# Kernel optimization log

Measured on AMD Instinct MI355X. Metric: run time of the kernel, lower is better.

## Reference

```python
import jax, jax.numpy as jnp
import numpy as np

N_STATE = 4      # d_state from CrossMambaFusionBlock(d_state=4)
DT_RANK = 48     # ceil(768/16), standard Mamba dt_rank='auto'
D_CONV = 4       # depthwise causal conv kernel size


def _ln(x, g, b):
    m = jnp.mean(x, axis=-1, keepdims=True)
    v = jnp.mean((x - m) ** 2, axis=-1, keepdims=True)
    return (x - m) * jax.lax.rsqrt(v + 1e-5) * g + b


def _dwconv1d(u, w, b):
    # u: (B,L,D); w: (D,1,K) depthwise causal conv along token dim L
    K = w.shape[-1]
    up = jnp.pad(jnp.transpose(u, (0, 2, 1)), ((0, 0), (0, 0), (K - 1, 0)))
    out = jax.lax.conv_general_dilated(up, w, (1,), 'VALID',
                                       feature_group_count=w.shape[0],
                                       dimension_numbers=('NCH', 'OIH', 'NCH'))
    return jnp.transpose(out, (0, 2, 1)) + b


def _pre(x, g, b, Win, Wconv, bconv, Wxp, Wdt, bdt):
    # LayerNorm -> in_proj -> depthwise conv + SiLU -> dt/B/C projections
    B_, H, W, C = x.shape
    xn = _ln(x, g, b).reshape(B_, H * W, C)
    u, z = jnp.split(xn @ Win, 2, axis=-1)              # (B,L,D) each
    u = jax.nn.silu(_dwconv1d(u, Wconv, bconv))
    dbl = u @ Wxp                                        # (B,L,R+2N)
    dtr, Bm, Cm = jnp.split(dbl, [DT_RANK, DT_RANK + N_STATE], axis=-1)
    dt = jax.nn.softplus(dtr @ Wdt + bdt)                # (B,L,D)
    return u, z, dt, Bm, Cm


def _selective_scan(u, dt, Alog, Bm, Cm, Dskip):
    # u, dt: (B,L,D); Alog: (D,N); Bm, Cm: (B,L,N)
    A = -jnp.exp(Alog)
    dA = jnp.exp(dt[..., None] * A)                      # (B,L,D,N) decay
    dBu = (dt * u)[..., None] * Bm[:, :, None, :]        # (B,L,D,N) input

    def comb(c1, c2):
        a1, h1 = c1
        a2, h2 = c2
        return a1 * a2, a2 * h1 + h2

    _, h = jax.lax.associative_scan(comb, (dA, dBu), axis=1)
    return jnp.einsum('bldn,bln->bld', h, Cm) + u * Dskip


def _forward(x1, x2,
             ln_g1, ln_b1, Win1, Wconv1, bconv1, Wxp1, Wdt1, bdt1, Alog1, Dskip1, Wout1,
             ln_g2, ln_b2, Win2, Wconv2, bconv2, Wxp2, Wdt2, bdt2, Alog2, Dskip2, Wout2):
    x1 = jnp.transpose(x1, (0, 2, 3, 1))  # BCHW -> BHWC (as in forward_features)
    x2 = jnp.transpose(x2, (0, 2, 3, 1))
    B_, H, W, C = x1.shape
    u1, z1, dt1, B1, C1 = _pre(x1, ln_g1, ln_b1, Win1, Wconv1, bconv1, Wxp1, Wdt1, bdt1)
    u2, z2, dt2, B2, C2 = _pre(x2, ln_g2, ln_b2, Win2, Wconv2, bconv2, Wxp2, Wdt2, bdt2)
    # Cross-modal fusion: each stream's SSM state is read out with the OTHER
    # stream's C projection (cross selective scan).
    y1 = _selective_scan(u1, dt1, Alog1, B1, C2, Dskip1)
    y2 = _selective_scan(u2, dt2, Alog2, B2, C1, Dskip2)
    o1 = ((y1 * jax.nn.silu(z1)) @ Wout1).reshape(B_, H, W, C)
    o2 = ((y2 * jax.nn.silu(z2)) @ Wout2).reshape(B_, H, W, C)
    return x1 + o1, x2 + o2


def setup_inputs():
    key = jax.random.key(0)
    ks = jax.random.split(key, 16)
    B_, C, H, W = 2, 768, 64, 64
    D = C  # d_inner (ssm_ratio = 1)

    def nrm(k, shape, s=0.02):
        return jax.random.normal(k, shape, jnp.float32) * s

    inp = {
        'x1': jax.random.normal(ks[0], (B_, C, H, W), jnp.float32),
        'x2': jax.random.normal(ks[1], (B_, C, H, W), jnp.float32),
    }
    for i, o in ((1, 2), (2, 8)):
        inp[f'ln_g{i}'] = jnp.ones((C,), jnp.float32)
        inp[f'ln_b{i}'] = jnp.zeros((C,), jnp.float32)
        inp[f'Win{i}'] = nrm(ks[o], (C, 2 * D))
        inp[f'Wconv{i}'] = nrm(ks[o + 1], (D, 1, D_CONV), 0.1)
        inp[f'bconv{i}'] = jnp.zeros((D,), jnp.float32)
        inp[f'Wxp{i}'] = nrm(ks[o + 2], (D, DT_RANK + 2 * N_STATE))
        inp[f'Wdt{i}'] = nrm(ks[o + 3], (DT_RANK, D), 0.05)
        inp[f'bdt{i}'] = jnp.full((D,), -4.6, jnp.float32)  # softplus -> dt ~ 0.01
        inp[f'Alog{i}'] = jnp.log(jnp.broadcast_to(
            jnp.arange(1, N_STATE + 1, dtype=jnp.float32), (D, N_STATE)))
        inp[f'Dskip{i}'] = jnp.ones((D,), jnp.float32)
        inp[f'Wout{i}'] = nrm(ks[o + 4], (D, C))
    return inp


def reference(x1, x2,
              ln_g1, ln_b1, Win1, Wconv1, bconv1, Wxp1, Wdt1, bdt1, Alog1, Dskip1, Wout1,
              ln_g2, ln_b2, Win2, Wconv2, bconv2, Wxp2, Wdt2, bdt2, Alog2, Dskip2, Wout2):
    return _forward(x1, x2,
                    ln_g1, ln_b1, Win1, Wconv1, bconv1, Wxp1, Wdt1, bdt1, Alog1, Dskip1, Wout1,
                    ln_g2, ln_b2, Win2, Wconv2, bconv2, Wxp2, Wdt2, bdt2, Alog2, Dskip2, Wout2)
```

## Files before the change

kernel.cpp:

```cpp
#include <hip/hip_runtime.h>
#include <cmath>

#define LDIM 4096
#define CDIM 768
#define BDIM 2
#define NST 4
#define RNK 48
#define CH 64
#define LC 64
#define NDT 896

typedef short bf16x8 __attribute__((ext_vector_type(8)));
typedef float f32x4 __attribute__((ext_vector_type(4)));

__device__ __forceinline__ float sigmoidf_(float x) { return 1.f / (1.f + __expf(-x)); }

__device__ __forceinline__ unsigned short f2bf(float f) {
    unsigned int u = __float_as_uint(f);
    u += 0x7fffu + ((u >> 16) & 1u);
    return (unsigned short)(u >> 16);
}
__device__ __forceinline__ float bf2f(unsigned short us) {
    unsigned int u = ((unsigned int)us) << 16;
    return __uint_as_float(u);
}
__device__ __forceinline__ float bf2f_lo(unsigned int p) { return __uint_as_float(p << 16); }
__device__ __forceinline__ float bf2f_hi(unsigned int p) { return __uint_as_float(p & 0xffff0000u); }

__device__ __forceinline__ void llds16(const unsigned short* g, unsigned short* l) {
    __builtin_amdgcn_global_load_lds(
        (const __attribute__((address_space(1))) unsigned int*)g,
        (__attribute__((address_space(3))) unsigned int*)l, 16, 0, 0);
}

__global__ __launch_bounds__(256) void prep_kernel(
    const float* __restrict__ x0, const float* __restrict__ x1, float* __restrict__ stats,
    const float* __restrict__ Win0, const float* __restrict__ Win1,
    const float* __restrict__ Wout0, const float* __restrict__ Wout1,
    unsigned short* __restrict__ WinT0, unsigned short* __restrict__ WinT1,
    unsigned short* __restrict__ WoutT0, unsigned short* __restrict__ WoutT1,
    const float* __restrict__ Wxp0, const float* __restrict__ Wdt0,
    const float* __restrict__ Wxp1, const float* __restrict__ Wdt1,
    unsigned short* __restrict__ Wc0, unsigned short* __restrict__ Wc1)
{
    __shared__ float smem[64 * 65];
    int bid = blockIdx.x;
    int t = threadIdx.x;

    if (bid < 256) {
        int s = bid >> 7;
        int b = (bid >> 6) & 1;
        int l0 = (bid & 63) * 64;
        int wave = t >> 6, lane = t & 63;
        const float* x = s ? x1 : x0;
        const float* xp = x + ((size_t)b * CDIM) * LDIM + l0 + lane;
        float sm = 0.f, sq = 0.f;
        int cbeg = wave * 192;
#pragma unroll
        for (int i0 = 0; i0 < 192; i0 += 16) {
            float v[16];
#pragma unroll
            for (int j = 0; j < 16; j++) v[j] = xp[(size_t)(cbeg + i0 + j) * LDIM];
#pragma unroll
            for (int j = 0; j < 16; j++) { sm += v[j]; sq += v[j] * v[j]; }
        }
        float* red = smem;
        red[(0 * 4 + wave) * 64 + lane] = sm;
        red[(1 * 4 + wave) * 64 + lane] = sq;
        __syncthreads();
        if (wave == 0) {
            float s_ = red[lane] + red[64 + lane] + red[128 + lane] + red[192 + lane];
            float q_ = red[256 + lane] + red[320 + lane] + red[384 + lane] + red[448 + lane];
            float m = s_ * (1.f / CDIM);
            float var = q_ * (1.f / CDIM) - m * m;
            int idx = s * 8192 + b * LDIM + l0 + lane;
            stats[2 * idx] = m;
            stats[2 * idx + 1] = rsqrtf(var + 1e-5f);
        }
        return;
    }
    if (bid < 1408) {
        int b2 = bid - 256;
        int bx = b2 % 24, by = (b2 / 24) % 12, z = b2 / 288;
        const float* W = (z == 0) ? Win0 : (z == 1) ? Win1 : (z == 2) ? Wout0 : Wout1;
        unsigned short* Wt = (z == 0) ? WinT0 : (z == 1) ? WinT1 : (z == 2) ? WoutT0 : WoutT1;
        const int K = CDIM;
        const int N = (z < 2) ? 2 * CDIM : CDIM;
        if (bx * 64 >= N) return;
        float (*tile)[65] = (float(*)[65])smem;
        int n0 = bx * 64, k0 = by * 64;
        int tn = t & 63, tg = t >> 6;
#pragma unroll
        for (int i = 0; i < 16; i++) {
            int kl = tg * 16 + i;
            tile[kl][tn] = W[(size_t)(k0 + kl) * N + n0 + tn];
        }
        __syncthreads();
#pragma unroll
        for (int i = 0; i < 16; i++) {
            int nl = tg * 16 + i;
            int k = k0 + tn, n = n0 + nl;
            Wt[(size_t)n * K + k] = f2bf(tile[tn][nl]);
        }
        return;
    }
    {
        int b3 = bid - 1408;
        int bx = b3 % 12, by = (b3 / 12) % 14, s = b3 / 168;
        const float* Wxp = s ? Wxp1 : Wxp0;
        const float* Wdt = s ? Wdt1 : Wdt0;
        unsigned short* WcombT = s ? Wc1 : Wc0;
        int k = bx * 64 + (t & 63);
        int n0 = by * 64;
        float wx[RNK];
#pragma unroll
        for (int r = 0; r < RNK; r++) wx[r] = Wxp[k * 56 + r];
        for (int i = (t >> 6); i < 64; i += 4) {
            int n = n0 + i;
            float val;
            if (n < CDIM) {
                float acc = 0.f;
#pragma unroll
                for (int r = 0; r < RNK; r++) acc += wx[r] * Wdt[(size_t)r * CDIM + n];
                val = acc;
            } else if (n < CDIM + 8) {
                val = Wxp[k * 56 + RNK + (n - CDIM)];
            } else {
                val = 0.f;
            }
            WcombT[(size_t)n * CDIM + k] = f2bf(val);
        }
    }
}

__global__ __launch_bounds__(256) void transpose_ln_kernel(
    const float* __restrict__ x0, const float* __restrict__ x1,
    const float* __restrict__ g0, const float* __restrict__ bb0,
    const float* __restrict__ g1, const float* __restrict__ bb1,
    const float* __restrict__ stats,
    unsigned short* __restrict__ xnb0, unsigned short* __restrict__ xnb1,
    float* __restrict__ out)
{
    __shared__ float tile[64][65];
    int t = threadIdx.x;
    int c0 = blockIdx.x * 64, l0 = blockIdx.y * 64;
    int z = blockIdx.z;
    int s = z >> 1, b = z & 1;
    const float* x = s ? x1 : x0;
    const float* g = s ? g1 : g0;
    const float* bb = s ? bb1 : bb0;
    unsigned short* xnb = s ? xnb1 : xnb0;
    int lane16 = t & 15, cg = t >> 4;
#pragma unroll
    for (int i = 0; i < 4; i++) {
        int cl = cg + 16 * i;
        f32x4 v = *(const f32x4*)&x[((size_t)(b * CDIM + c0 + cl)) * LDIM + l0 + lane16 * 4];
#pragma unroll
        for (int j = 0; j < 4; j++) tile[cl][lane16 * 4 + j] = v[j];
    }
    __syncthreads();
    const size_t SZ = (size_t)BDIM * LDIM * CDIM;
    int tl = t & 63, tg = t >> 6;
#pragma unroll
    for (int i = 0; i < 16; i++) {
        int ll = tg * 16 + i;
        int l = l0 + ll, c = c0 + tl;
        float v = tile[tl][ll];
        int sidx = s * 8192 + b * LDIM + l;
        float m = stats[sidx * 2], rs = stats[sidx * 2 + 1];
        size_t o = ((size_t)(b * LDIM + l)) * CDIM + c;
        out[(size_t)s * SZ + o] = v;
        xnb[o] = f2bf((v - m) * rs * g[c] + bb[c]);
    }
}

__global__ __launch_bounds__(512, 4) void gemm_mfma(
    const unsigned short* __restrict__ A0, const unsigned short* __restrict__ A1,
    const unsigned short* __restrict__ Bt0, const unsigned short* __restrict__ Bt1,
    void* __restrict__ C0, void* __restrict__ C1, int ldc, int K, int epi,
    const float* __restrict__ bias0, const float* __restrict__ bias1,
    float* __restrict__ D0, float* __restrict__ D1)
{
    const unsigned short* A = blockIdx.z ? A1 : A0;
    const unsigned short* Bt = blockIdx.z ? Bt1 : Bt0;
    void* C = blockIdx.z ? C1 : C0;
    const float* bias = blockIdx.z ? bias1 : bias0;
    float* D = blockIdx.z ? D1 : D0;

    __shared__ unsigned short As[3][128 * 32];
    __shared__ unsigned short Bs[3][128 * 32];
    const int tid = threadIdx.x;
    const int wave = tid >> 6, lane = tid & 63;
    const int row0 = blockIdx.x * 128, col0 = blockIdx.y * 128;
    const int wm = (wave >> 2) * 64, wn = (wave & 3) * 32;
    f32x4 acc[4][2] = {};
    const int lr = lane >> 2;
    const int gi = ((lane & 3) ^ ((lane >> 3) & 3)) * 8;
    const int fr = lane & 15, fc = lane >> 4;

    const unsigned short* ga0 = A + (size_t)(row0 + wave * 16 + lr) * K + gi;
    const unsigned short* gb0 = Bt + (size_t)(col0 + wave * 16 + lr) * K + gi;
    const int rb = wave * 16;

#define ISSUE(st, kb)                         \
    do {                                      \
        llds16(ga0 + (kb), &As[st][rb * 32]); \
        llds16(gb0 + (kb), &Bs[st][rb * 32]); \
    } while (0)

    const int NIT = K / 32;
    ISSUE(0, 0);
    ISSUE(1, 32);
    for (int i = 0; i < NIT; i++) {
        if (i < NIT - 1) __builtin_amdgcn_s_waitcnt(0xF72);
        else __builtin_amdgcn_s_waitcnt(0xF70);
        __builtin_amdgcn_s_barrier();
        if (i + 2 < NIT) ISSUE((i + 2) % 3, (i + 2) * 32);
        const unsigned short* as = As[i % 3];
        const unsigned short* bs = Bs[i % 3];
        bf16x8 af[4], bfr[2];
#pragma unroll
        for (int ii = 0; ii < 4; ii++) {
            int r = wm + ii * 16 + fr;
            af[ii] = *(const bf16x8*)&as[r * 32 + (fc ^ ((r >> 1) & 3)) * 8];
        }
#pragma unroll
        for (int j = 0; j < 2; j++) {
            int r = wn + j * 16 + fr;
            bfr[j] = *(const bf16x8*)&bs[r * 32 + (fc ^ ((r >> 1) & 3)) * 8];
        }
#pragma unroll
        for (int ii = 0; ii < 4; ii++)
#pragma unroll
            for (int j = 0; j < 2; j++)
                acc[ii][j] = __builtin_amdgcn_mfma_f32_16x16x32_bf16(af[ii], bfr[j], acc[ii][j], 0, 0, 0);
    }
#undef ISSUE

    const int cr = (lane >> 4) * 4, cc = lane & 15;
#pragma unroll
    for (int ii = 0; ii < 4; ii++)
#pragma unroll
        for (int j = 0; j < 2; j++) {
            int col = col0 + wn + j * 16 + cc;
#pragma unroll
            for (int r = 0; r < 4; r++) {
                int row = row0 + wm + ii * 16 + cr + r;
                float v = acc[ii][j][r];
                if (epi == 1) {
                    float* Cf = (float*)C;
                    size_t o = (size_t)row * ldc + col;
                    Cf[o] = v + Cf[o];
                } else if (epi == 2) {
                    if (col < CDIM) {
                        v += bias[col];
                        v = (v > 20.f) ? v : __logf(1.f + __expf(v));
                        ((unsigned short*)C)[(size_t)row * ldc + col] = f2bf(v);
                    } else if (col < CDIM + 8) {
                        D[(size_t)row * 8 + (col - CDIM)] = v;
                    }
                } else {
                    ((unsigned short*)C)[(size_t)row * ldc + col] = f2bf(v);
                }
            }
        }
}

__global__ __launch_bounds__(256) void conv_silu_kernel(
    const unsigned short* __restrict__ uzb0, const unsigned short* __restrict__ uzb1,
    const float* __restrict__ w0, const float* __restrict__ bc0,
    const float* __restrict__ w1, const float* __restrict__ bc1,
    unsigned short* __restrict__ ub0, unsigned short* __restrict__ ub1)
{
    int s = blockIdx.y;
    const unsigned short* uzb = s ? uzb1 : uzb0;
    const float* w = s ? w1 : w0;
    const float* bc = s ? bc1 : bc0;
    unsigned short* ub = s ? ub1 : ub0;
    int idx = blockIdx.x * 256 + threadIdx.x;
    int d8 = (idx % 96) * 8;
    int bl = idx / 96;
    int l = bl & (LDIM - 1);

    float wr[8][4];
#pragma unroll
    for (int q = 0; q < 8; q++) {
        f32x4 wv = *(const f32x4*)&w[(d8 + q) * 4];
#pragma unroll
        for (int k = 0; k < 4; k++) wr[q][k] = wv[k];
    }
    float acc[8];
    f32x4 b0 = *(const f32x4*)&bc[d8];
    f32x4 b1 = *(const f32x4*)&bc[d8 + 4];
#pragma unroll
    for (int q = 0; q < 4; q++) { acc[q] = b0[q]; acc[4 + q] = b1[q]; }

#pragma unroll
    for (int k = 0; k < 4; k++) {
        int ls = l - 3 + k;
        if (ls >= 0) {
            bf16x8 uv = *(const bf16x8*)&uzb[(size_t)(bl - 3 + k) * (2 * CDIM) + d8];
#pragma unroll
            for (int q = 0; q < 8; q++)
                acc[q] += bf2f((unsigned short)uv[q]) * wr[q][k];
        }
    }
    bf16x8 ov;
#pragma unroll
    for (int q = 0; q < 8; q++) {
        float v = acc[q];
        ov[q] = (short)f2bf(v * sigmoidf_(v));
    }
    *(bf16x8*)&ub[(size_t)bl * CDIM + d8] = ov;
}

__global__ __launch_bounds__(256) void scan_phaseA(
    const unsigned short* __restrict__ u0, const unsigned short* __restrict__ dt0,
    const float* __restrict__ dbl0, const float* __restrict__ Alog0,
    const unsigned short* __restrict__ u1, const unsigned short* __restrict__ dt1,
    const float* __restrict__ dbl1, const float* __restrict__ Alog1,
    float* __restrict__ agg)
{
    int idx = blockIdx.x * 256 + threadIdx.x;
    int dp = idx % 384;
    int d0 = dp * 2;
    int t1 = idx / 384;
    int c = t1 % CH;
    int t2 = t1 / CH;
    int b = t2 & 1;
    int s = t2 >> 1;
    const unsigned short* u = s ? u1 : u0;
    const unsigned short* dt = s ? dt1 : dt0;
    const float* dbl = s ? dbl1 : dbl0;
    const float* Alog = s ? Alog1 : Alog0;
    float A[2][4];
#pragma unroll
    for (int j = 0; j < 2; j++)
#pragma unroll
        for (int n = 0; n < 4; n++) A[j][n] = -__expf(Alog[(d0 + j) * 4 + n]);
    float h[2][4] = {}, aa[2][4];
#pragma unroll
    for (int j = 0; j < 2; j++)
#pragma unroll
        for (int n = 0; n < 4; n++) aa[j][n] = 1.f;
    int rowb = b * LDIM + c * LC;
    for (int t = 0; t < LC; t++) {
        int row = rowb + t;
        unsigned int up = *(const unsigned int*)&u[(size_t)row * CDIM + d0];
        unsigned int dp2 = *(const unsigned int*)&dt[(size_t)row * CDIM + d0];
        float uv[2] = {bf2f_lo(up), bf2f_hi(up)};
        float dtv[2] = {bf2f_lo(dp2), bf2f_hi(dp2)};
        const float* bm = dbl + (size_t)row * 8;
#pragma unroll
        for (int j = 0; j < 2; j++) {
            float du = dtv[j] * uv[j];
#pragma unroll
            for (int n = 0; n < 4; n++) {
                float dA = __expf(dtv[j] * A[j][n]);
                h[j][n] = dA * h[j][n] + du * bm[n];
                aa[j][n] *= dA;
            }
        }
    }
    size_t base = ((size_t)(s * 2 + b) * CH + c) * CDIM + d0;
#pragma unroll
    for (int j = 0; j < 2; j++) {
        float* o = agg + (base + j) * 8;
#pragma unroll
        for (int n = 0; n < 4; n++) { o[n] = aa[j][n]; o[4 + n] = h[j][n]; }
    }
}

__global__ __launch_bounds__(256) void scan_phaseB(const float* __restrict__ agg,
                                                   float* __restrict__ hinit)
{
    int idx = blockIdx.x * 256 + threadIdx.x;
    int d = idx % CDIM;
    int sb = idx / CDIM;
    float st[4] = {0, 0, 0, 0};
    for (int c = 0; c < CH; c++) {
        size_t base = ((size_t)sb * CH + c) * CDIM + d;
        const float* a = agg + base * 8;
        float* hi = hinit + base * 4;
#pragma unroll
        for (int n = 0; n < 4; n++) hi[n] = st[n];
#pragma unroll
        for (int n = 0; n < 4; n++) st[n] = a[n] * st[n] + a[4 + n];
    }
}

__global__ __launch_bounds__(256) void scan_phaseC(
    const unsigned short* __restrict__ u0, const unsigned short* __restrict__ dt0,
    const unsigned short* __restrict__ uzb0, const float* __restrict__ dbl0,
    const float* __restrict__ Alog0, const float* __restrict__ Dsk0, unsigned short* __restrict__ g0,
    const unsigned short* __restrict__ u1, const unsigned short* __restrict__ dt1,
    const unsigned short* __restrict__ uzb1, const float* __restrict__ dbl1,
    const float* __restrict__ Alog1, const float* __restrict__ Dsk1, unsigned short* __restrict__ g1,
    const float* __restrict__ hinit)
{
    int idx = blockIdx.x * 256 + threadIdx.x;
    int dp = idx % 384;
    int d0 = dp * 2;
    int t1 = idx / 384;
    int c = t1 % CH;
    int t2 = t1 / CH;
    int b = t2 & 1;
    int s = t2 >> 1;
    const unsigned short* u = s ? u1 : u0;
    const unsigned short* dt = s ? dt1 : dt0;
    const unsigned short* uzb = s ? uzb1 : uzb0;
    const float* dbl = s ? dbl1 : dbl0;
    const float* dblO = s ? dbl0 : dbl1;
    const float* Alog = s ? Alog1 : Alog0;
    const float* Dsk = s ? Dsk1 : Dsk0;
    unsigned short* gated = s ? g1 : g0;
    float A[2][4];
#pragma unroll
    for (int j = 0; j < 2; j++)
#pragma unroll
        for (int n = 0; n < 4; n++) A[j][n] = -__expf(Alog[(d0 + j) * 4 + n]);
    float Dv[2] = {Dsk[d0], Dsk[d0 + 1]};
    float h[2][4];
    size_t base = ((size_t)(s * 2 + b) * CH + c) * CDIM + d0;
#pragma unroll
    for (int j = 0; j < 2; j++) {
        const float* hi = hinit + (base + j) * 4;
#pragma unroll
        for (int n = 0; n < 4; n++) h[j][n] = hi[n];
    }
    int rowb = b * LDIM + c * LC;
    for (int t = 0; t < LC; t++) {
        int row = rowb + t;
        unsigned int up = *(const unsigned int*)&u[(size_t)row * CDIM + d0];
        unsigned int dp2 = *(const unsigned int*)&dt[(size_t)row * CDIM + d0];
        unsigned int zp = *(const unsigned int*)&uzb[(size_t)row * (2 * CDIM) + CDIM + d0];
        float uv[2] = {bf2f_lo(up), bf2f_hi(up)};
        float dtv[2] = {bf2f_lo(dp2), bf2f_hi(dp2)};
        float zv[2] = {bf2f_lo(zp), bf2f_hi(zp)};
        const float* bm = dbl + (size_t)row * 8;
        const float* cm = dblO + (size_t)row * 8 + 4;
        unsigned int outp = 0;
#pragma unroll
        for (int j = 0; j < 2; j++) {
            float du = dtv[j] * uv[j];
            float y = 0.f;
#pragma unroll
            for (int n = 0; n < 4; n++) {
                float dA = __expf(dtv[j] * A[j][n]);
                h[j][n] = dA * h[j][n] + du * bm[n];
                y += h[j][n] * cm[n];
            }
            y += uv[j] * Dv[j];
            unsigned short gb = f2bf(y * (zv[j] * sigmoidf_(zv[j])));
            outp |= ((unsigned int)gb) << (16 * j);
        }
        *(unsigned int*)&gated[(size_t)row * CDIM + d0] = outp;
    }
}

extern "C" void kernel_launch(void* const* d_in, const int* in_sizes, int n_in,
                              void* d_out, int out_size, void* d_ws, size_t ws_size,
                              hipStream_t stream)
{
    const float* x[2] = {(const float*)d_in[0], (const float*)d_in[1]};
    const float *ln_g[2], *ln_b[2], *Win[2], *Wconv[2], *bconv[2], *Wxp[2],
        *Wdt[2], *bdt[2], *Alog[2], *Dskip[2], *Wout[2];
    for (int s = 0; s < 2; s++) {
        int base = 2 + s * 11;
        ln_g[s] = (const float*)d_in[base + 0];
        ln_b[s] = (const float*)d_in[base + 1];
        Win[s] = (const float*)d_in[base + 2];
        Wconv[s] = (const float*)d_in[base + 3];
        bconv[s] = (const float*)d_in[base + 4];
        Wxp[s] = (const float*)d_in[base + 5];
        Wdt[s] = (const float*)d_in[base + 6];
        bdt[s] = (const float*)d_in[base + 7];
        Alog[s] = (const float*)d_in[base + 8];
        Dskip[s] = (const float*)d_in[base + 9];
        Wout[s] = (const float*)d_in[base + 10];
    }

    const int M = BDIM * LDIM;
    char* base = (char*)d_ws;
    auto alloc = [&](size_t bytes) {
        char* p = base;
        base += (bytes + 255) & ~(size_t)255;
        return p;
    };
    unsigned short* uzb[2] = {(unsigned short*)alloc((size_t)M * 1536 * 2),
                              (unsigned short*)alloc((size_t)M * 1536 * 2)};
    unsigned short* dtb[2] = {(unsigned short*)alloc((size_t)M * CDIM * 2),
                              (unsigned short*)alloc((size_t)M * CDIM * 2)};
    unsigned short* ub[2] = {(unsigned short*)alloc((size_t)M * CDIM * 2),
                             (unsigned short*)alloc((size_t)M * CDIM * 2)};
    unsigned short* xnb[2] = {(unsigned short*)alloc((size_t)M * CDIM * 2),
                              (unsigned short*)alloc((size_t)M * CDIM * 2)};
    float* dbl[2] = {(float*)alloc((size_t)M * 8 * 4), (float*)alloc((size_t)M * 8 * 4)};
    unsigned short* WinT[2] = {(unsigned short*)alloc(1536 * 768 * 2),
                               (unsigned short*)alloc(1536 * 768 * 2)};
    unsigned short* WoutT[2] = {(unsigned short*)alloc(768 * 768 * 2),
                                (unsigned short*)alloc(768 * 768 * 2)};
    unsigned short* WcombT[2] = {(unsigned short*)alloc((size_t)NDT * 768 * 2),
                                 (unsigned short*)alloc((size_t)NDT * 768 * 2)};
    float* agg = (float*)alloc((size_t)2 * BDIM * CH * CDIM * 8 * 4);
    float* hinit = (float*)alloc((size_t)2 * BDIM * CH * CDIM * 4 * 4);
    float* stats = (float*)alloc((size_t)2 * M * 2 * 4);

    dim3 blk(256);
    dim3 blk512(512);
    const size_t SZ = (size_t)BDIM * LDIM * CDIM;

    prep_kernel<<<dim3(1744), blk, 0, stream>>>(
        x[0], x[1], stats,
        Win[0], Win[1], Wout[0], Wout[1], WinT[0], WinT[1], WoutT[0], WoutT[1],
        Wxp[0], Wdt[0], Wxp[1], Wdt[1], WcombT[0], WcombT[1]);

    transpose_ln_kernel<<<dim3(CDIM / 64, LDIM / 64, 4), blk, 0, stream>>>(
        x[0], x[1], ln_g[0], ln_b[0], ln_g[1], ln_b[1], stats, xnb[0], xnb[1], (float*)d_out);

    gemm_mfma<<<dim3(M / 128, 1536 / 128, 2), blk512, 0, stream>>>(
        xnb[0], xnb[1], WinT[0], WinT[1], uzb[0], uzb[1], 2 * CDIM, CDIM, 3,
        nullptr, nullptr, nullptr, nullptr);

    conv_silu_kernel<<<dim3((M * CDIM / 8) / 256, 2), blk, 0, stream>>>(
        uzb[0], uzb[1], Wconv[0], bconv[0], Wconv[1], bconv[1], ub[0], ub[1]);

    gemm_mfma<<<dim3(M / 128, NDT / 128, 2), blk512, 0, stream>>>(
        ub[0], ub[1], WcombT[0], WcombT[1], dtb[0], dtb[1], CDIM, CDIM, 2,
        bdt[0], bdt[1], dbl[0], dbl[1]);

    scan_phaseA<<<dim3((2 * BDIM * CH * (CDIM / 2)) / 256), blk, 0, stream>>>(
        ub[0], dtb[0], dbl[0], Alog[0], ub[1], dtb[1], dbl[1], Alog[1], agg);
    scan_phaseB<<<dim3((2 * BDIM * CDIM) / 256), blk, 0, stream>>>(agg, hinit);
    scan_phaseC<<<dim3((2 * BDIM * CH * (CDIM / 2)) / 256), blk, 0, stream>>>(
        ub[0], dtb[0], uzb[0], dbl[0], Alog[0], Dskip[0], xnb[0],
        ub[1], dtb[1], uzb[1], dbl[1], Alog[1], Dskip[1], xnb[1], hinit);

    float* out = (float*)d_out;
    gemm_mfma<<<dim3(M / 128, CDIM / 128, 2), blk512, 0, stream>>>(
        xnb[0], xnb[1], WoutT[0], WoutT[1], out, out + SZ, CDIM, CDIM, 1,
        nullptr, nullptr, nullptr, nullptr);
}
```

Measured before the change: 423.7 us.

## Vectorize transpose-LN stores, reuse conv rows across tokens, parallelize scan phase B

The transpose/LayerNorm kernel now writes four channels per thread as f32x4 and bf16x4 vector stores and loads gamma/beta once per thread. The conv+SiLU kernel computes four consecutive tokens per thread, sharing seven loaded rows instead of reloading four per token, and launches a quarter as many threads. Scan phase B assigns one thread per state element instead of one per channel, giving it four times more parallelism for its serial chunk loop. Together these target memory-transaction overhead and low occupancy in three small kernels. In exchange, the transposed tile reads may hit more LDS bank conflicts, and phase B now issues narrower scattered loads.

```diff
diff --git a/kernel.cpp b/kernel.cpp
--- a/kernel.cpp
+++ b/kernel.cpp
@@ -11,6 +11,7 @@
 #define NDT 896
 
 typedef short bf16x8 __attribute__((ext_vector_type(8)));
+typedef short bf16x4 __attribute__((ext_vector_type(4)));
 typedef float f32x4 __attribute__((ext_vector_type(4)));
 
 __device__ __forceinline__ float sigmoidf_(float x) { return 1.f / (1.f + __expf(-x)); }
@@ -160,17 +161,26 @@
     }
     __syncthreads();
     const size_t SZ = (size_t)BDIM * LDIM * CDIM;
-    int tl = t & 63, tg = t >> 6;
-#pragma unroll
-    for (int i = 0; i < 16; i++) {
-        int ll = tg * 16 + i;
-        int l = l0 + ll, c = c0 + tl;
-        float v = tile[tl][ll];
+    int c4 = (t & 15) * 4, lg = t >> 4;
+    f32x4 gv = *(const f32x4*)&g[c0 + c4];
+    f32x4 bv = *(const f32x4*)&bb[c0 + c4];
+#pragma unroll
+    for (int i = 0; i < 4; i++) {
+        int ll = lg + 16 * i;
+        int l = l0 + ll;
         int sidx = s * 8192 + b * LDIM + l;
         float m = stats[sidx * 2], rs = stats[sidx * 2 + 1];
-        size_t o = ((size_t)(b * LDIM + l)) * CDIM + c;
-        out[(size_t)s * SZ + o] = v;
-        xnb[o] = f2bf((v - m) * rs * g[c] + bb[c]);
+        f32x4 rv;
+        bf16x4 nv;
+#pragma unroll
+        for (int j = 0; j < 4; j++) {
+            float v = tile[c4 + j][ll];
+            rv[j] = v;
+            nv[j] = (short)f2bf((v - m) * rs * gv[j] + bv[j]);
+        }
+        size_t o = ((size_t)(b * LDIM + l)) * CDIM + c0 + c4;
+        *(f32x4*)&out[(size_t)s * SZ + o] = rv;
+        *(bf16x4*)&xnb[o] = nv;
     }
 }
 
@@ -279,8 +289,8 @@
     unsigned short* ub = s ? ub1 : ub0;
     int idx = blockIdx.x * 256 + threadIdx.x;
     int d8 = (idx % 96) * 8;
-    int bl = idx / 96;
-    int l = bl & (LDIM - 1);
+    int bl0 = (idx / 96) * 4;
+    int l0 = bl0 & (LDIM - 1);
 
     float wr[8][4];
 #pragma unroll
@@ -289,29 +299,38 @@
 #pragma unroll
         for (int k = 0; k < 4; k++) wr[q][k] = wv[k];
     }
-    float acc[8];
     f32x4 b0 = *(const f32x4*)&bc[d8];
     f32x4 b1 = *(const f32x4*)&bc[d8 + 4];
-#pragma unroll
-    for (int q = 0; q < 4; q++) { acc[q] = b0[q]; acc[4 + q] = b1[q]; }
-
-#pragma unroll
-    for (int k = 0; k < 4; k++) {
-        int ls = l - 3 + k;
-        if (ls >= 0) {
-            bf16x8 uv = *(const bf16x8*)&uzb[(size_t)(bl - 3 + k) * (2 * CDIM) + d8];
+
+    bf16x8 rows[7];
+#pragma unroll
+    for (int j = 0; j < 7; j++) {
+        int ls = l0 - 3 + j;
+        if (ls >= 0)
+            rows[j] = *(const bf16x8*)&uzb[(size_t)(bl0 - 3 + j) * (2 * CDIM) + d8];
+        else
+            rows[j] = bf16x8{};
+    }
+
+#pragma unroll
+    for (int li = 0; li < 4; li++) {
+        float acc[8];
+#pragma unroll
+        for (int q = 0; q < 4; q++) { acc[q] = b0[q]; acc[4 + q] = b1[q]; }
+#pragma unroll
+        for (int k = 0; k < 4; k++) {
 #pragma unroll
             for (int q = 0; q < 8; q++)
-                acc[q] += bf2f((unsigned short)uv[q]) * wr[q][k];
-        }
-    }
-    bf16x8 ov;
-#pragma unroll
-    for (int q = 0; q < 8; q++) {
-        float v = acc[q];
-        ov[q] = (short)f2bf(v * sigmoidf_(v));
-    }
-    *(bf16x8*)&ub[(size_t)bl * CDIM + d8] = ov;
+                acc[q] += bf2f((unsigned short)rows[li + k][q]) * wr[q][k];
+        }
+        bf16x8 ov;
+#pragma unroll
+        for (int q = 0; q < 8; q++) {
+            float v = acc[q];
+            ov[q] = (short)f2bf(v * sigmoidf_(v));
+        }
+        *(bf16x8*)&ub[(size_t)(bl0 + li) * CDIM + d8] = ov;
+    }
 }
 
 __global__ __launch_bounds__(256) void scan_phaseA(
@@ -375,17 +394,14 @@
                                                    float* __restrict__ hinit)
 {
     int idx = blockIdx.x * 256 + threadIdx.x;
-    int d = idx % CDIM;
-    int sb = idx / CDIM;
-    float st[4] = {0, 0, 0, 0};
+    int n = idx & 3;
+    int d = (idx >> 2) % CDIM;
+    int sb = idx / (CDIM * 4);
+    float st = 0.f;
     for (int c = 0; c < CH; c++) {
         size_t base = ((size_t)sb * CH + c) * CDIM + d;
-        const float* a = agg + base * 8;
-        float* hi = hinit + base * 4;
-#pragma unroll
-        for (int n = 0; n < 4; n++) hi[n] = st[n];
-#pragma unroll
-        for (int n = 0; n < 4; n++) st[n] = a[n] * st[n] + a[4 + n];
+        hinit[base * 4 + n] = st;
+        st = agg[base * 8 + n] * st + agg[base * 8 + 4 + n];
     }
 }
 
@@ -522,7 +538,7 @@
         xnb[0], xnb[1], WinT[0], WinT[1], uzb[0], uzb[1], 2 * CDIM, CDIM, 3,
         nullptr, nullptr, nullptr, nullptr);
 
-    conv_silu_kernel<<<dim3((M * CDIM / 8) / 256, 2), blk, 0, stream>>>(
+    conv_silu_kernel<<<dim3((M * CDIM / 32) / 256, 2), blk, 0, stream>>>(
         uzb[0], uzb[1], Wconv[0], bconv[0], Wconv[1], bconv[1], ub[0], ub[1]);
 
     gemm_mfma<<<dim3(M / 128, NDT / 128, 2), blk512, 0, stream>>>(
@@ -531,7 +547,7 @@
 
     scan_phaseA<<<dim3((2 * BDIM * CH * (CDIM / 2)) / 256), blk, 0, stream>>>(
         ub[0], dtb[0], dbl[0], Alog[0], ub[1], dtb[1], dbl[1], Alog[1], agg);
-    scan_phaseB<<<dim3((2 * BDIM * CDIM) / 256), blk, 0, stream>>>(agg, hinit);
+    scan_phaseB<<<dim3((2 * BDIM * CDIM * 4) / 256), blk, 0, stream>>>(agg, hinit);
     scan_phaseC<<<dim3((2 * BDIM * CH * (CDIM / 2)) / 256), blk, 0, stream>>>(
         ub[0], dtb[0], uzb[0], dbl[0], Alog[0], Dskip[0], xnb[0],
         ub[1], dtb[1], uzb[1], dbl[1], Alog[1], Dskip[1], xnb[1], hinit);
```

New measurement: 404.5 us. 4.5% less time.
